# Kernel optimization log

Hardware: AMD Instinct MI355X
Metric: run time of the kernel (lower is better)

Reference implementation:

```python
import jax, jax.numpy as jnp
import numpy as np

B, T, D = 4, 4096, 2048
NE = 64
TOP_K = 8


def setup_inputs() -> dict:
    key = jax.random.key(0)
    k1, k2 = jax.random.split(key)
    x = jax.random.normal(k1, (B, T, D), dtype=jnp.float32)
    w = jax.random.normal(k2, (NE, D), dtype=jnp.float32) * (1.0 / np.sqrt(D))
    gate_b = jnp.zeros((NE,), dtype=jnp.float32)
    return {"x": x, "w": w, "gate_b": gate_b, "top_k": TOP_K}


def reference(x, w, gate_b, top_k):
    # router logits: [b, t, ne]
    logits = jnp.einsum('nd,btd->btn', w, x)
    scores = jax.nn.sigmoid(logits) + gate_b
    weights, indices = jax.lax.top_k(scores, top_k)
    weights = weights / weights.sum(-1, keepdims=True)
    return (weights, indices, scores)
```

## Files before the change

### kernel.cpp

```cpp
#include <hip/hip_runtime.h>
#include <math.h>

#define D_DIM 2048
#define NE    64
#define NTOK  16384
#define TK    8
#define TOKB  64
#define BT    512
#define CHD   64
#define NCHK  (D_DIM / CHD)
#define WCH   4096

#define RROW  68
#define SLICE (TOKB * RROW)
#define POOLF (4 * SLICE)

#define OUT_I_OFF (NTOK * TK)
#define OUT_S_OFF (2 * NTOK * TK)

#define GLOBAL_AS __attribute__((address_space(1)))
#define LDS_AS    __attribute__((address_space(3)))

static __device__ __forceinline__ void async_copy16(const float* g, float* l) {
    __builtin_amdgcn_global_load_lds((const GLOBAL_AS void*)g, (LDS_AS void*)l, 16, 0, 0);
}

__global__ __launch_bounds__(BT, 1) void gate_fused(const float* __restrict__ x,
                                                    const float* __restrict__ w,
                                                    const float* __restrict__ gb,
                                                    float* __restrict__ out) {
    __shared__ __align__(16) float pool[POOLF];

    float* scores = out + OUT_S_OFF;
    const int tid  = threadIdx.x;
    const int lane = tid & 63;
    const int ks   = tid >> 6;
    const int lt   = lane >> 3;
    const int le   = lane & 7;
    const int tok0 = blockIdx.x * TOKB;

    const int e0  = tid >> 4;
    const int qp0 = tid & 15;
    const float* src0 = w + (size_t)e0 * D_DIM + ((qp0 ^ (e0 & 7)) << 2);

    auto stage = [&](int c, int buf) {
        float* d = pool + buf * WCH + tid * 4;
        async_copy16(src0 + c * CHD, d);
        async_copy16(src0 + 32 * D_DIM + c * CHD, d + 2048);
    };

    const float4* xq[8];
#pragma unroll
    for (int i = 0; i < 8; ++i)
        xq[i] = (const float4*)x + (size_t)(tok0 + i * 8 + lt) * (D_DIM / 4);

    float acc[8][8];
#pragma unroll
    for (int i = 0; i < 8; ++i)
#pragma unroll
        for (int j = 0; j < 8; ++j) acc[i][j] = 0.f;

    stage(0, 0);

    for (int c = 0; c < NCHK; ++c) {
        __syncthreads();
        if (c + 1 < NCHK) stage(c + 1, (c + 1) & 1);
        const float* wb = pool + (c & 1) * WCH;
#pragma unroll
        for (int qq = 0; qq < 2; ++qq) {
            const int qL = ks * 2 + qq;
            float4 xi[8];
#pragma unroll
            for (int i = 0; i < 8; ++i) xi[i] = xq[i][c * 16 + qL];
            float4 wj[8];
#pragma unroll
            for (int j = 0; j < 8; ++j)
                wj[j] = *(const float4*)(wb + (j * 8 + le) * 64 + ((qL ^ le) << 2));
#pragma unroll
            for (int i = 0; i < 8; ++i) {
#pragma unroll
                for (int j = 0; j < 8; ++j) {
                    acc[i][j] = fmaf(xi[i].x, wj[j].x, acc[i][j]);
                    acc[i][j] = fmaf(xi[i].y, wj[j].y, acc[i][j]);
                    acc[i][j] = fmaf(xi[i].z, wj[j].z, acc[i][j]);
                    acc[i][j] = fmaf(xi[i].w, wj[j].w, acc[i][j]);
                }
            }
        }
    }

    __syncthreads();
    if (ks >= 4) {
        float* pr = pool + (ks - 4) * SLICE;
#pragma unroll
        for (int i = 0; i < 8; ++i)
#pragma unroll
            for (int j = 0; j < 8; ++j)
                pr[(i * 8 + lt) * RROW + j * 8 + le] = acc[i][j];
    }
    __syncthreads();
    if (ks < 4) {
        float* pr = pool + ks * SLICE;
#pragma unroll
        for (int i = 0; i < 8; ++i)
#pragma unroll
            for (int j = 0; j < 8; ++j)
                pr[(i * 8 + lt) * RROW + j * 8 + le] += acc[i][j];
    }
    __syncthreads();
#pragma unroll
    for (int k = 0; k < 2; ++k) {
        const int v  = k * 512 + tid;
        const int t  = v >> 4;
        const int e4 = v & 15;
        float4 s = {0.f, 0.f, 0.f, 0.f};
#pragma unroll
        for (int sl = 0; sl < 4; ++sl) {
            float4 a = *(const float4*)(pool + sl * SLICE + t * RROW + e4 * 4);
            s.x += a.x; s.y += a.y; s.z += a.z; s.w += a.w;
        }
        float4 g = *(const float4*)(gb + e4 * 4);
        float4 r;
        r.x = 1.f / (1.f + expf(-s.x)) + g.x;
        r.y = 1.f / (1.f + expf(-s.y)) + g.y;
        r.z = 1.f / (1.f + expf(-s.z)) + g.z;
        r.w = 1.f / (1.f + expf(-s.w)) + g.w;
        *(float4*)(scores + (size_t)(tok0 + t) * NE + e4 * 4) = r;
        *(float4*)(pool + t * RROW + e4 * 4) = r;
    }
    __syncthreads();

    if (tid < 256) {
        const int t  = tid >> 2;
        const int q4 = tid & 3;
        float v[16];
        const float4* sp = (const float4*)(pool + t * RROW + q4 * 16);
        float4 a = sp[0], b = sp[1], c = sp[2], d = sp[3];
        v[0] = a.x;  v[1] = a.y;  v[2] = a.z;  v[3] = a.w;
        v[4] = b.x;  v[5] = b.y;  v[6] = b.z;  v[7] = b.w;
        v[8] = c.x;  v[9] = c.y;  v[10] = c.z; v[11] = c.w;
        v[12] = d.x; v[13] = d.y; v[14] = d.z; v[15] = d.w;

        float kv[TK]; int ki[TK];
#pragma unroll
        for (int k = 0; k < TK; ++k) {
            float bv = v[0]; int bi = q4 * 16;
#pragma unroll
            for (int j = 1; j < 16; ++j) {
                bool gt = v[j] > bv;
                bv = gt ? v[j] : bv;
                bi = gt ? (q4 * 16 + j) : bi;
            }
#pragma unroll
            for (int off = 1; off < 4; off <<= 1) {
                float ov = __shfl_xor(bv, off);
                int   oi = __shfl_xor(bi, off);
                bool take = (ov > bv) || (ov == bv && oi < bi);
                bv = take ? ov : bv;
                bi = take ? oi : bi;
            }
            int lj = bi - q4 * 16;
#pragma unroll
            for (int j = 0; j < 16; ++j) v[j] = (j == lj) ? -3e38f : v[j];
            kv[k] = bv; ki[k] = bi;
        }

        if (q4 == 0) {
            float s = 0.f;
#pragma unroll
            for (int k = 0; k < TK; ++k) s += kv[k];
            float inv = 1.f / s;
            float* ow = out + (size_t)(tok0 + t) * TK;
            float* oi = out + OUT_I_OFF + (size_t)(tok0 + t) * TK;
#pragma unroll
            for (int k = 0; k < TK; ++k) {
                ow[k] = kv[k] * inv;
                oi[k] = (float)ki[k];
            }
        }
    }
}

extern "C" void kernel_launch(void* const* d_in, const int* in_sizes, int n_in,
                              void* d_out, int out_size, void* d_ws, size_t ws_size,
                              hipStream_t stream) {
    const float* x  = (const float*)d_in[0];
    const float* w  = (const float*)d_in[1];
    const float* gb = (const float*)d_in[2];
    float* out = (float*)d_out;
    (void)in_sizes; (void)n_in; (void)out_size; (void)d_ws; (void)ws_size;

    gate_fused<<<dim3(NTOK / TOKB), dim3(BT), 0, stream>>>(x, w, gb, out);
}
```

Measured before the change: 257.2 us.

## Double W chunk depth and software-pipeline register loads of x and w

Doubles the staged weight chunk along D from 64 to 128 floats, so the main loop runs half as many iterations and block barriers. Each thread now stages four async 16-byte copies per chunk. The inner loop uses two alternating register sets for x and w fragments: the next quad's global x load and LDS w load are issued before the FMAs on the current quad. The first x fragment of the next chunk is prefetched across the barrier. This aims to hide global and LDS latency behind the FMAs, at the cost of more VGPRs and a larger LDS footprint.

```diff
diff --git a/kernel.cpp b/kernel.cpp
--- a/kernel.cpp
+++ b/kernel.cpp
@@ -7,9 +7,10 @@
 #define TK    8
 #define TOKB  64
 #define BT    512
-#define CHD   64
+#define CHD   128
 #define NCHK  (D_DIM / CHD)
-#define WCH   4096
+#define NQR   (CHD / 4)
+#define WCH   (NE * CHD)
 
 #define RROW  68
 #define SLICE (TOKB * RROW)
@@ -39,14 +40,19 @@
     const int le   = lane & 7;
     const int tok0 = blockIdx.x * TOKB;
 
-    const int e0  = tid >> 4;
-    const int qp0 = tid & 15;
-    const float* src0 = w + (size_t)e0 * D_DIM + ((qp0 ^ (e0 & 7)) << 2);
+    const int e0  = tid >> 5;
+    const int qp0 = tid & 31;
+    const int dq0 = qp0 ^ (e0 & 7);
+    const float* srcq[4];
+#pragma unroll
+    for (int k = 0; k < 4; ++k)
+        srcq[k] = w + (size_t)(e0 + 16 * k) * D_DIM + (dq0 << 2);
 
     auto stage = [&](int c, int buf) {
         float* d = pool + buf * WCH + tid * 4;
-        async_copy16(src0 + c * CHD, d);
-        async_copy16(src0 + 32 * D_DIM + c * CHD, d + 2048);
+#pragma unroll
+        for (int k = 0; k < 4; ++k)
+            async_copy16(srcq[k] + c * CHD, d + k * 2048);
     };
 
     const float4* xq[8];
@@ -60,33 +66,48 @@
 #pragma unroll
         for (int j = 0; j < 8; ++j) acc[i][j] = 0.f;
 
+    float4 xiA[8], xiB[8], wjA[8], wjB[8];
+    const int qL0 = ks * 4;
+
+    auto loadx = [&](float4 (&X)[8], int qidx) {
+#pragma unroll
+        for (int i = 0; i < 8; ++i) X[i] = xq[i][qidx];
+    };
+    auto loadw = [&](float4 (&W)[8], const float* wb, int qL) {
+#pragma unroll
+        for (int j = 0; j < 8; ++j)
+            W[j] = *(const float4*)(wb + (j * 8 + le) * CHD + ((qL ^ le) << 2));
+    };
+    auto fmas = [&](float4 (&X)[8], float4 (&W)[8]) {
+#pragma unroll
+        for (int i = 0; i < 8; ++i) {
+#pragma unroll
+            for (int j = 0; j < 8; ++j) {
+                acc[i][j] = fmaf(X[i].x, W[j].x, acc[i][j]);
+                acc[i][j] = fmaf(X[i].y, W[j].y, acc[i][j]);
+                acc[i][j] = fmaf(X[i].z, W[j].z, acc[i][j]);
+                acc[i][j] = fmaf(X[i].w, W[j].w, acc[i][j]);
+            }
+        }
+    };
+
     stage(0, 0);
+    loadx(xiA, qL0);
 
     for (int c = 0; c < NCHK; ++c) {
         __syncthreads();
         if (c + 1 < NCHK) stage(c + 1, (c + 1) & 1);
         const float* wb = pool + (c & 1) * WCH;
-#pragma unroll
-        for (int qq = 0; qq < 2; ++qq) {
-            const int qL = ks * 2 + qq;
-            float4 xi[8];
-#pragma unroll
-            for (int i = 0; i < 8; ++i) xi[i] = xq[i][c * 16 + qL];
-            float4 wj[8];
-#pragma unroll
-            for (int j = 0; j < 8; ++j)
-                wj[j] = *(const float4*)(wb + (j * 8 + le) * 64 + ((qL ^ le) << 2));
-#pragma unroll
-            for (int i = 0; i < 8; ++i) {
-#pragma unroll
-                for (int j = 0; j < 8; ++j) {
-                    acc[i][j] = fmaf(xi[i].x, wj[j].x, acc[i][j]);
-                    acc[i][j] = fmaf(xi[i].y, wj[j].y, acc[i][j]);
-                    acc[i][j] = fmaf(xi[i].z, wj[j].z, acc[i][j]);
-                    acc[i][j] = fmaf(xi[i].w, wj[j].w, acc[i][j]);
-                }
-            }
-        }
+        const int qb = c * NQR + qL0;
+        loadw(wjA, wb, qL0);
+        loadx(xiB, qb + 1); loadw(wjB, wb, qL0 + 1);
+        fmas(xiA, wjA);
+        loadx(xiA, qb + 2); loadw(wjA, wb, qL0 + 2);
+        fmas(xiB, wjB);
+        loadx(xiB, qb + 3); loadw(wjB, wb, qL0 + 3);
+        fmas(xiA, wjA);
+        if (c + 1 < NCHK) loadx(xiA, (c + 1) * NQR + qL0);
+        fmas(xiB, wjB);
     }
 
     __syncthreads();
```

New measurement: 650.1 us. 2.53x slower.
